# Kernel tuning notes

Measured on AMD Instinct MI355X. Metric: run time of the kernel, lower is better.

Reference implementation:

```python
import jax, jax.numpy as jnp
import numpy as np

V, E, H, L = 32000, 1024, 1024, 2  # vocab, embed, hidden, num_layers
START_TOKEN = 0


def setup_inputs() -> dict:
    key = jax.random.key(0)
    ks = jax.random.split(key, 10)
    s = 1.0 / np.sqrt(H)
    return {
        "encoder_outputs": jax.random.normal(ks[0], (64, 32, H), jnp.float32),
        "encoder_hidden": jax.random.normal(ks[1], (L, 64, H), jnp.float32),
        "emb": jax.random.normal(ks[2], (V, E), jnp.float32) * s,
        "w_ih": jax.random.normal(ks[3], (L, 3 * H, E), jnp.float32) * s,
        "w_hh": jax.random.normal(ks[4], (L, 3 * H, H), jnp.float32) * s,
        "b_ih": jax.random.normal(ks[5], (L, 3 * H), jnp.float32) * s,
        "b_hh": jax.random.normal(ks[6], (L, 3 * H), jnp.float32) * s,
        "out_w": jax.random.normal(ks[7], (V, H), jnp.float32) * s,
        "out_b": jax.random.normal(ks[8], (V,), jnp.float32) * s,
        "max_length": 32,
    }


def _gru_cell(x, h, wi, wh, bi, bh):
    # torch GRU gate order: r, z, n
    gi = x @ wi.T + bi          # [B, 3H]
    gh = h @ wh.T + bh          # [B, 3H]
    ir, iz, inn = jnp.split(gi, 3, axis=-1)
    hr, hz, hn = jnp.split(gh, 3, axis=-1)
    r = jax.nn.sigmoid(ir + hr)
    z = jax.nn.sigmoid(iz + hz)
    n = jnp.tanh(inn + r * hn)
    return (1.0 - z) * n + z * h


def reference(encoder_outputs, encoder_hidden, emb, w_ih, w_hh, b_ih, b_hh,
              out_w, out_b, max_length):
    B = encoder_outputs.shape[0]
    tok0 = jnp.full((B,), START_TOKEN, dtype=jnp.int32)

    def step(carry, _):
        h, tok = carry                      # h: [L,B,H], tok: [B]
        x = jax.nn.relu(emb[tok])           # embedding + (dropout p=0) + relu
        new_h = []
        for l in range(L):
            hl = _gru_cell(x, h[l], w_ih[l], w_hh[l], b_ih[l], b_hh[l])
            new_h.append(hl)
            x = hl
        h = jnp.stack(new_h)
        logits = x @ out_w.T + out_b        # [B, V]
        tok = jnp.argmax(logits, axis=-1).astype(jnp.int32)  # topk(1), detached
        return (h, tok), logits

    (h_final, _), logits = jax.lax.scan(step, (encoder_hidden, tok0), None,
                                        length=max_length)
    decoder_outputs = jnp.transpose(logits, (1, 0, 2))  # [B, T, V]
    return decoder_outputs, h_final
```

## Files before the change

kernel.cpp:

```cpp
#include <hip/hip_runtime.h>
#include <math.h>
#include <float.h>


#define B_ 64
#define H_ 1024
#define V_ 32000
#define T_ 32

typedef unsigned short u16;
typedef float f32x4 __attribute__((ext_vector_type(4)));
typedef short s16x8 __attribute__((ext_vector_type(8)));
#define MFMA16 __builtin_amdgcn_mfma_f32_16x16x32_bf16

#define WOH_B   0UL
#define WOL_B   65536000UL
#define WIHH_B  131072000UL
#define WIHL_B  143654912UL
#define WHHH_B  156237824UL
#define WHHL_B  168820736UL
#define XH_B    181403648UL
#define XL_B    181534720UL
#define HBH_B   181665792UL
#define HBL_B   181927936UL
#define HF_B    182190080UL
#define GT_B    182714368UL
#define PV_B    184287232UL
#define PI_B    184543232UL
#define TK_B    184799232UL

#define OUT_H_OFF 65536000L

__device__ __forceinline__ void bf16split(float x, u16& h, u16& l) {
  unsigned u = __float_as_uint(x);
  unsigned r = u + 0x7fff + ((u >> 16) & 1);
  h = (u16)(r >> 16);
  float hf = __uint_as_float((unsigned)h << 16);
  float rem = x - hf;
  unsigned u2 = __float_as_uint(rem);
  unsigned r2 = u2 + 0x7fff + ((u2 >> 16) & 1);
  l = (u16)(r2 >> 16);
}

__global__ void k_convert(const float* __restrict__ src, u16* __restrict__ hi,
                          u16* __restrict__ lo, int n4) {
  int i = blockIdx.x * 256 + threadIdx.x;
  int stride = gridDim.x * 256;
  for (; i < n4; i += stride) {
    float4 v = ((const float4*)src)[i];
    float x[4] = {v.x, v.y, v.z, v.w};
    u16 hh[4], ll[4];
    #pragma unroll
    for (int j = 0; j < 4; ++j) bf16split(x[j], hh[j], ll[j]);
    ushort4 ho; ho.x = hh[0]; ho.y = hh[1]; ho.z = hh[2]; ho.w = hh[3];
    ushort4 lv; lv.x = ll[0]; lv.y = ll[1]; lv.z = ll[2]; lv.w = ll[3];
    ((ushort4*)hi)[i] = ho;
    ((ushort4*)lo)[i] = lv;
  }
}

__global__ void k_init(const float* __restrict__ enc_h, float* __restrict__ hf,
                       u16* __restrict__ hhi, u16* __restrict__ hlo,
                       int* __restrict__ tok) {
  int n = blockIdx.x * 256 + threadIdx.x;
  float v = enc_h[n];
  hf[n] = v;
  u16 h, l; bf16split(v, h, l);
  hhi[n] = h; hlo[n] = l;
  if (n < B_) tok[n] = 0;
}

__global__ void k_argmax_embed(const float* __restrict__ emb,
                               const float* __restrict__ pv, const int* __restrict__ pidx,
                               int* __restrict__ tok, u16* __restrict__ xhi,
                               u16* __restrict__ xlo, int do_argmax) {
  __shared__ float sv[1024];
  __shared__ int   si[1024];
  int tid = threadIdx.x;
  if (do_argmax) {
    int b = tid & 63, c = tid >> 6;
    float best = -FLT_MAX; int bi = 0x7fffffff;
    for (int i = c; i < 1000; i += 16) {
      float v = pv[i * 64 + b];
      int  ix = pidx[i * 64 + b];
      if (v > best || (v == best && ix < bi)) { best = v; bi = ix; }
    }
    sv[c * 64 + b] = best; si[c * 64 + b] = bi;
    __syncthreads();
    if (tid < 64) {
      float bv = sv[tid]; int bix = si[tid];
      #pragma unroll
      for (int c2 = 1; c2 < 16; ++c2) {
        float v2 = sv[c2 * 64 + tid]; int i2 = si[c2 * 64 + tid];
        if (v2 > bv || (v2 == bv && i2 < bix)) { bv = v2; bix = i2; }
      }
      tok[tid] = bix;
    }
  }
  __syncthreads();
  int b = tid >> 4, tl = tid & 15;
  const float* erow = emb + (long)tok[b] * H_;
  #pragma unroll
  for (int c = 0; c < 16; ++c) {
    int e = c * 64 + tl * 4;
    float4 v = *(const float4*)(erow + e);
    float x0 = fmaxf(v.x, 0.f), x1 = fmaxf(v.y, 0.f);
    float x2 = fmaxf(v.z, 0.f), x3 = fmaxf(v.w, 0.f);
    u16 h0,h1,h2,h3,l0,l1,l2,l3;
    bf16split(x0,h0,l0); bf16split(x1,h1,l1); bf16split(x2,h2,l2); bf16split(x3,h3,l3);
    ushort4 hv; hv.x=h0; hv.y=h1; hv.z=h2; hv.w=h3;
    ushort4 lv; lv.x=l0; lv.y=l1; lv.z=l2; lv.w=l3;
    *(ushort4*)(xhi + b * 1024 + e) = hv;
    *(ushort4*)(xlo + b * 1024 + e) = lv;
  }
}

__device__ __forceinline__ void gemm32x64_slice(
    const u16* __restrict__ Ahi, const u16* __restrict__ Alo,
    const u16* __restrict__ Bhi, const u16* __restrict__ Blo,
    int lane, int kbeg, f32x4 (&acc)[2][4]) {
  int l15 = lane & 15, l4 = lane >> 4;
  const u16* pah = Ahi + l15 * 1024 + l4 * 8 + kbeg;
  const u16* pal = Alo + l15 * 1024 + l4 * 8 + kbeg;
  const u16* pbh = Bhi + l15 * 1024 + l4 * 8 + kbeg;
  const u16* pbl = Blo + l15 * 1024 + l4 * 8 + kbeg;
  #pragma unroll 2
  for (int k0 = 0; k0 < 256; k0 += 32) {
    s16x8 ah0 = *(const s16x8*)(pah + k0);
    s16x8 ah1 = *(const s16x8*)(pah + 16 * 1024 + k0);
    s16x8 al0 = *(const s16x8*)(pal + k0);
    s16x8 al1 = *(const s16x8*)(pal + 16 * 1024 + k0);
    #pragma unroll
    for (int nt = 0; nt < 4; ++nt) {
      s16x8 bh = *(const s16x8*)(pbh + nt * 16 * 1024 + k0);
      s16x8 bl = *(const s16x8*)(pbl + nt * 16 * 1024 + k0);
      acc[0][nt] = MFMA16(ah0, bh, acc[0][nt], 0, 0, 0);
      acc[1][nt] = MFMA16(ah1, bh, acc[1][nt], 0, 0, 0);
      acc[0][nt] = MFMA16(ah0, bl, acc[0][nt], 0, 0, 0);
      acc[1][nt] = MFMA16(ah1, bl, acc[1][nt], 0, 0, 0);
      acc[0][nt] = MFMA16(al0, bh, acc[0][nt], 0, 0, 0);
      acc[1][nt] = MFMA16(al1, bh, acc[1][nt], 0, 0, 0);
    }
  }
}

__global__ __launch_bounds__(256) void k_gru(
    const u16* __restrict__ aih_hi, const u16* __restrict__ aih_lo,
    const u16* __restrict__ ahh_hi, const u16* __restrict__ ahh_lo,
    const float* __restrict__ bih, const float* __restrict__ bhh,
    const u16* __restrict__ xb_hi, const u16* __restrict__ xb_lo,
    const u16* __restrict__ hb_hi, const u16* __restrict__ hb_lo,
    float* __restrict__ gt) {
  __shared__ f32x4 sacc[4][64][5];
  int tid = threadIdx.x;
  int wave = tid >> 6, lane = tid & 63;
  int l15 = lane & 15, l4 = lane >> 4;
  int blk = blockIdx.x;
  bool ih = blk < 96;
  int row0 = (ih ? blk : blk - 96) * 32;
  const u16* Ahi = (ih ? aih_hi : ahh_hi) + (size_t)row0 * 1024;
  const u16* Alo = (ih ? aih_lo : ahh_lo) + (size_t)row0 * 1024;
  const u16* Bhi = ih ? xb_hi : hb_hi;
  const u16* Blo = ih ? xb_lo : hb_lo;
  const float* bias = (ih ? bih : bhh) + row0;
  f32x4 acc[2][4];
  #pragma unroll
  for (int m = 0; m < 2; ++m)
    #pragma unroll
    for (int n = 0; n < 4; ++n) acc[m][n] = (f32x4){0.f, 0.f, 0.f, 0.f};
  gemm32x64_slice(Ahi, Alo, Bhi, Blo, lane, wave * 256, acc);
  #pragma unroll
  for (int nt = 0; nt < 4; ++nt) sacc[wave][lane][nt] = acc[0][nt];
  __syncthreads();
  f32x4 s0 = sacc[0][lane][wave];
  #pragma unroll
  for (int j = 1; j < 4; ++j) s0 += sacc[j][lane][wave];
  __syncthreads();
  #pragma unroll
  for (int nt = 0; nt < 4; ++nt) sacc[wave][lane][nt] = acc[1][nt];
  __syncthreads();
  f32x4 s1 = sacc[0][lane][wave];
  #pragma unroll
  for (int j = 1; j < 4; ++j) s1 += sacc[j][lane][wave];
  int grow0 = (ih ? 0 : 3072) + row0;
  int b = wave * 16 + l15;
  f32x4 bs0 = *(const f32x4*)(bias + l4 * 4);
  f32x4 bs1 = *(const f32x4*)(bias + 16 + l4 * 4);
  *(f32x4*)(gt + (size_t)b * 6144 + grow0 + l4 * 4) = s0 + bs0;
  *(f32x4*)(gt + (size_t)b * 6144 + grow0 + 16 + l4 * 4) = s1 + bs1;
}

__global__ void k_gates(const float* __restrict__ gt, float* __restrict__ hf,
                        u16* __restrict__ hhi, u16* __restrict__ hlo) {
  int n = blockIdx.x * 256 + threadIdx.x;
  int b = n >> 10, j = n & 1023;
  const float* gb = gt + (size_t)b * 6144;
  float ir = gb[j], iz = gb[j + 1024], inn = gb[j + 2048];
  float hr = gb[j + 3072], hz = gb[j + 4096], hn = gb[j + 5120];
  float r = 1.f / (1.f + expf(-(ir + hr)));
  float z = 1.f / (1.f + expf(-(iz + hz)));
  float nn = tanhf(inn + r * hn);
  float ho = hf[n];
  float hv = (1.f - z) * nn + z * ho;
  hf[n] = hv;
  u16 hh, ll; bf16split(hv, hh, ll);
  hhi[n] = hh; hlo[n] = ll;
}

__global__ __launch_bounds__(256) void k_logits(
    const u16* __restrict__ whi, const u16* __restrict__ wlo,
    const float* __restrict__ bo, const u16* __restrict__ xhi,
    const u16* __restrict__ xlo, float* __restrict__ pv, int* __restrict__ pidx,
    float* __restrict__ dout, int t) {
  __shared__ f32x4 sacc[4][64][5];
  int tid = threadIdx.x;
  int wave = tid >> 6, lane = tid & 63;
  int l15 = lane & 15, l4 = lane >> 4;
  int v0 = blockIdx.x * 32;
  f32x4 acc[2][4];
  #pragma unroll
  for (int m = 0; m < 2; ++m)
    #pragma unroll
    for (int n = 0; n < 4; ++n) acc[m][n] = (f32x4){0.f, 0.f, 0.f, 0.f};
  gemm32x64_slice(whi + (size_t)v0 * 1024, wlo + (size_t)v0 * 1024,
                  xhi, xlo, lane, wave * 256, acc);
  #pragma unroll
  for (int nt = 0; nt < 4; ++nt) sacc[wave][lane][nt] = acc[0][nt];
  __syncthreads();
  f32x4 s0 = sacc[0][lane][wave];
  #pragma unroll
  for (int j = 1; j < 4; ++j) s0 += sacc[j][lane][wave];
  __syncthreads();
  #pragma unroll
  for (int nt = 0; nt < 4; ++nt) sacc[wave][lane][nt] = acc[1][nt];
  __syncthreads();
  f32x4 s1 = sacc[0][lane][wave];
  #pragma unroll
  for (int j = 1; j < 4; ++j) s1 += sacc[j][lane][wave];
  long b = wave * 16 + l15;
  f32x4 out0 = s0 + *(const f32x4*)(bo + v0 + l4 * 4);
  f32x4 out1 = s1 + *(const f32x4*)(bo + v0 + 16 + l4 * 4);
  float* addr = dout + b * (T_ * (long)V_) + (long)t * V_ + v0 + l4 * 4;
  __builtin_nontemporal_store(out0, (f32x4*)addr);
  __builtin_nontemporal_store(out1, (f32x4*)(addr + 16));
  float bv = -FLT_MAX; int bi = 0;
  #pragma unroll
  for (int r = 0; r < 4; ++r) {
    float v = out0[r];
    if (v > bv) { bv = v; bi = v0 + l4 * 4 + r; }
  }
  #pragma unroll
  for (int r = 0; r < 4; ++r) {
    float v = out1[r];
    if (v > bv) { bv = v; bi = v0 + 16 + l4 * 4 + r; }
  }
  #pragma unroll
  for (int off = 16; off < 64; off <<= 1) {
    float ov = __shfl_xor(bv, off, 64);
    int   oi = __shfl_xor(bi, off, 64);
    if (ov > bv || (ov == bv && oi < bi)) { bv = ov; bi = oi; }
  }
  if (l4 == 0) {
    pv[blockIdx.x * 64 + wave * 16 + l15] = bv;
    pidx[blockIdx.x * 64 + wave * 16 + l15] = bi;
  }
}

__global__ void k_final(const float* __restrict__ hf, float* __restrict__ dout) {
  int n = blockIdx.x * 256 + threadIdx.x;
  dout[OUT_H_OFF + n] = hf[n];
}

extern "C" void kernel_launch(void* const* d_in, const int* in_sizes, int n_in,
                              void* d_out, int out_size, void* d_ws, size_t ws_size,
                              hipStream_t stream) {
  const float* enc_h = (const float*)d_in[1];
  const float* emb   = (const float*)d_in[2];
  const float* w_ih  = (const float*)d_in[3];
  const float* w_hh  = (const float*)d_in[4];
  const float* b_ih  = (const float*)d_in[5];
  const float* b_hh  = (const float*)d_in[6];
  const float* out_w = (const float*)d_in[7];
  const float* out_b = (const float*)d_in[8];
  float* out = (float*)d_out;
  char* wsb = (char*)d_ws;

  u16* woh  = (u16*)(wsb + WOH_B);
  u16* wol  = (u16*)(wsb + WOL_B);
  u16* wihh = (u16*)(wsb + WIHH_B);
  u16* wihl = (u16*)(wsb + WIHL_B);
  u16* whhh = (u16*)(wsb + WHHH_B);
  u16* whhl = (u16*)(wsb + WHHL_B);
  u16* xh   = (u16*)(wsb + XH_B);
  u16* xl   = (u16*)(wsb + XL_B);
  u16* hbh  = (u16*)(wsb + HBH_B);
  u16* hbl  = (u16*)(wsb + HBL_B);
  float* hf = (float*)(wsb + HF_B);
  float* gt = (float*)(wsb + GT_B);
  float* pv = (float*)(wsb + PV_B);
  int* pidx = (int*)(wsb + PI_B);
  int* tok  = (int*)(wsb + TK_B);

  k_convert<<<4096, 256, 0, stream>>>(out_w, woh, wol, 8192000);
  k_convert<<<2048, 256, 0, stream>>>(w_ih, wihh, wihl, 1572864);
  k_convert<<<2048, 256, 0, stream>>>(w_hh, whhh, whhl, 1572864);
  k_init<<<512, 256, 0, stream>>>(enc_h, hf, hbh, hbl, tok);

  for (int t = 0; t < T_; ++t) {
    k_argmax_embed<<<1, 1024, 0, stream>>>(emb, pv, pidx, tok, xh, xl, t > 0);
    for (int l = 0; l < 2; ++l) {
      const u16* bxh = (l == 0) ? xh : hbh;
      const u16* bxl = (l == 0) ? xl : hbl;
      k_gru<<<192, 256, 0, stream>>>(wihh + (size_t)l * 3145728, wihl + (size_t)l * 3145728,
                                     whhh + (size_t)l * 3145728, whhl + (size_t)l * 3145728,
                                     b_ih + l * 3072, b_hh + l * 3072,
                                     bxh, bxl, hbh + l * 65536, hbl + l * 65536, gt);
      k_gates<<<256, 256, 0, stream>>>(gt, hf + l * 65536, hbh + l * 65536, hbl + l * 65536);
    }
    k_logits<<<1000, 256, 0, stream>>>(woh, wol, out_b, hbh + 65536, hbl + 65536,
                                       pv, pidx, out, t);
  }
  k_final<<<512, 256, 0, stream>>>(hf, out);
}
```

Before: 3.794 ms.

## Stage weight tiles into LDS via global_load_lds with 8-wave K split

The GEMM helper is restructured so each of 8 waves (512 threads) handles a 128-wide K slice. Each wave preloads its activation fragments into registers and streams the weight tile (hi and lo) directly into LDS with global_load_lds before running the MFMAs. The cross-wave reduction becomes a single 8-way LDS sum done by the first 4 waves. The goal is more bytes in flight per block and less latency for the bandwidth-bound weight streaming. In exchange each block uses 128 KB of LDS, which caps occupancy at one block per CU, and register pressure rises from the 32 preloaded B fragments.

New measurement: 4.001 ms. 5.5% more time.

```diff
diff --git a/kernel.cpp b/kernel.cpp
--- a/kernel.cpp
+++ b/kernel.cpp
@@ -42,6 +42,12 @@
   l = (u16)(r2 >> 16);
 }
 
+__device__ __forceinline__ void ld_g2l(void* lptr, const void* gptr) {
+  __builtin_amdgcn_global_load_lds(
+      (const __attribute__((address_space(1))) void*)gptr,
+      (__attribute__((address_space(3))) void*)lptr, 16, 0, 0);
+}
+
 __global__ void k_convert(const float* __restrict__ src, u16* __restrict__ hi,
                           u16* __restrict__ lo, int n4) {
   int i = blockIdx.x * 256 + threadIdx.x;
@@ -80,6 +86,7 @@
   if (do_argmax) {
     int b = tid & 63, c = tid >> 6;
     float best = -FLT_MAX; int bi = 0x7fffffff;
+    #pragma unroll 4
     for (int i = c; i < 1000; i += 16) {
       float v = pv[i * 64 + b];
       int  ix = pidx[i * 64 + b];
@@ -115,51 +122,65 @@
   }
 }
 
-__device__ __forceinline__ void gemm32x64_slice(
+__device__ __forceinline__ void stage_gemm32x64(
     const u16* __restrict__ Ahi, const u16* __restrict__ Alo,
     const u16* __restrict__ Bhi, const u16* __restrict__ Blo,
-    int lane, int kbeg, f32x4 (&acc)[2][4]) {
+    char* wslice, int wave, int lane, f32x4 (&acc)[2][4]) {
   int l15 = lane & 15, l4 = lane >> 4;
-  const u16* pah = Ahi + l15 * 1024 + l4 * 8 + kbeg;
-  const u16* pal = Alo + l15 * 1024 + l4 * 8 + kbeg;
-  const u16* pbh = Bhi + l15 * 1024 + l4 * 8 + kbeg;
-  const u16* pbl = Blo + l15 * 1024 + l4 * 8 + kbeg;
-  #pragma unroll 2
-  for (int k0 = 0; k0 < 256; k0 += 32) {
-    s16x8 ah0 = *(const s16x8*)(pah + k0);
-    s16x8 ah1 = *(const s16x8*)(pah + 16 * 1024 + k0);
-    s16x8 al0 = *(const s16x8*)(pal + k0);
-    s16x8 al1 = *(const s16x8*)(pal + 16 * 1024 + k0);
+  const u16* pbh = Bhi + l15 * 1024 + l4 * 8 + wave * 128;
+  const u16* pbl = Blo + l15 * 1024 + l4 * 8 + wave * 128;
+  s16x8 bh[4][4], bl[4][4];
+  #pragma unroll
+  for (int c = 0; c < 4; ++c)
     #pragma unroll
     for (int nt = 0; nt < 4; ++nt) {
-      s16x8 bh = *(const s16x8*)(pbh + nt * 16 * 1024 + k0);
-      s16x8 bl = *(const s16x8*)(pbl + nt * 16 * 1024 + k0);
-      acc[0][nt] = MFMA16(ah0, bh, acc[0][nt], 0, 0, 0);
-      acc[1][nt] = MFMA16(ah1, bh, acc[1][nt], 0, 0, 0);
-      acc[0][nt] = MFMA16(ah0, bl, acc[0][nt], 0, 0, 0);
-      acc[1][nt] = MFMA16(ah1, bl, acc[1][nt], 0, 0, 0);
-      acc[0][nt] = MFMA16(al0, bh, acc[0][nt], 0, 0, 0);
-      acc[1][nt] = MFMA16(al1, bh, acc[1][nt], 0, 0, 0);
-    }
-  }
-}
-
-__global__ __launch_bounds__(256) void k_gru(
+      bh[c][nt] = *(const s16x8*)(pbh + nt * 16384 + c * 32);
+      bl[c][nt] = *(const s16x8*)(pbl + nt * 16384 + c * 32);
+    }
+  {
+    int row = (lane >> 4);
+    int kof = (lane & 15) * 8;
+    #pragma unroll
+    for (int i = 0; i < 8; ++i) {
+      ld_g2l(wslice + i * 1024,        Ahi + (size_t)(i * 4 + row) * 1024 + kof);
+      ld_g2l(wslice + 8192 + i * 1024, Alo + (size_t)(i * 4 + row) * 1024 + kof);
+    }
+  }
+  __syncthreads();
+  #pragma unroll
+  for (int c = 0; c < 4; ++c) {
+    s16x8 ah0 = *(const s16x8*)(wslice + l15 * 256 + c * 64 + l4 * 16);
+    s16x8 ah1 = *(const s16x8*)(wslice + (l15 + 16) * 256 + c * 64 + l4 * 16);
+    s16x8 al0 = *(const s16x8*)(wslice + 8192 + l15 * 256 + c * 64 + l4 * 16);
+    s16x8 al1 = *(const s16x8*)(wslice + 8192 + (l15 + 16) * 256 + c * 64 + l4 * 16);
+    #pragma unroll
+    for (int nt = 0; nt < 4; ++nt) {
+      acc[0][nt] = MFMA16(ah0, bh[c][nt], acc[0][nt], 0, 0, 0);
+      acc[1][nt] = MFMA16(ah1, bh[c][nt], acc[1][nt], 0, 0, 0);
+      acc[0][nt] = MFMA16(ah0, bl[c][nt], acc[0][nt], 0, 0, 0);
+      acc[1][nt] = MFMA16(ah1, bl[c][nt], acc[1][nt], 0, 0, 0);
+      acc[0][nt] = MFMA16(al0, bh[c][nt], acc[0][nt], 0, 0, 0);
+      acc[1][nt] = MFMA16(al1, bh[c][nt], acc[1][nt], 0, 0, 0);
+    }
+  }
+}
+
+__global__ __launch_bounds__(512) void k_gru(
     const u16* __restrict__ aih_hi, const u16* __restrict__ aih_lo,
     const u16* __restrict__ ahh_hi, const u16* __restrict__ ahh_lo,
     const float* __restrict__ bih, const float* __restrict__ bhh,
     const u16* __restrict__ xb_hi, const u16* __restrict__ xb_lo,
     const u16* __restrict__ hb_hi, const u16* __restrict__ hb_lo,
     float* __restrict__ gt) {
-  __shared__ f32x4 sacc[4][64][5];
+  __shared__ __align__(16) char lds[131072];
   int tid = threadIdx.x;
   int wave = tid >> 6, lane = tid & 63;
   int l15 = lane & 15, l4 = lane >> 4;
   int blk = blockIdx.x;
   bool ih = blk < 96;
   int row0 = (ih ? blk : blk - 96) * 32;
-  const u16* Ahi = (ih ? aih_hi : ahh_hi) + (size_t)row0 * 1024;
-  const u16* Alo = (ih ? aih_lo : ahh_lo) + (size_t)row0 * 1024;
+  const u16* Ahi = (ih ? aih_hi : ahh_hi) + (size_t)row0 * 1024 + wave * 128;
+  const u16* Alo = (ih ? aih_lo : ahh_lo) + (size_t)row0 * 1024 + wave * 128;
   const u16* Bhi = ih ? xb_hi : hb_hi;
   const u16* Blo = ih ? xb_lo : hb_lo;
   const float* bias = (ih ? bih : bhh) + row0;
@@ -168,26 +189,30 @@
   for (int m = 0; m < 2; ++m)
     #pragma unroll
     for (int n = 0; n < 4; ++n) acc[m][n] = (f32x4){0.f, 0.f, 0.f, 0.f};
-  gemm32x64_slice(Ahi, Alo, Bhi, Blo, lane, wave * 256, acc);
-  #pragma unroll
-  for (int nt = 0; nt < 4; ++nt) sacc[wave][lane][nt] = acc[0][nt];
-  __syncthreads();
-  f32x4 s0 = sacc[0][lane][wave];
-  #pragma unroll
-  for (int j = 1; j < 4; ++j) s0 += sacc[j][lane][wave];
-  __syncthreads();
-  #pragma unroll
-  for (int nt = 0; nt < 4; ++nt) sacc[wave][lane][nt] = acc[1][nt];
-  __syncthreads();
-  f32x4 s1 = sacc[0][lane][wave];
-  #pragma unroll
-  for (int j = 1; j < 4; ++j) s1 += sacc[j][lane][wave];
-  int grow0 = (ih ? 0 : 3072) + row0;
-  int b = wave * 16 + l15;
-  f32x4 bs0 = *(const f32x4*)(bias + l4 * 4);
-  f32x4 bs1 = *(const f32x4*)(bias + 16 + l4 * 4);
-  *(f32x4*)(gt + (size_t)b * 6144 + grow0 + l4 * 4) = s0 + bs0;
-  *(f32x4*)(gt + (size_t)b * 6144 + grow0 + 16 + l4 * 4) = s1 + bs1;
+  stage_gemm32x64(Ahi, Alo, Bhi, Blo, lds + wave * 16384, wave, lane, acc);
+  __syncthreads();
+  f32x4* sa = (f32x4*)lds;
+  #pragma unroll
+  for (int mt = 0; mt < 2; ++mt)
+    #pragma unroll
+    for (int nt = 0; nt < 4; ++nt)
+      sa[(mt * 4 + nt) * 512 + wave * 64 + lane] = acc[mt][nt];
+  __syncthreads();
+  if (wave < 4) {
+    f32x4 s0 = sa[wave * 512 + lane];
+    f32x4 s1 = sa[(4 + wave) * 512 + lane];
+    #pragma unroll
+    for (int j = 1; j < 8; ++j) {
+      s0 += sa[wave * 512 + j * 64 + lane];
+      s1 += sa[(4 + wave) * 512 + j * 64 + lane];
+    }
+    int grow0 = (ih ? 0 : 3072) + row0;
+    int b = wave * 16 + l15;
+    f32x4 bs0 = *(const f32x4*)(bias + l4 * 4);
+    f32x4 bs1 = *(const f32x4*)(bias + 16 + l4 * 4);
+    *(f32x4*)(gt + (size_t)b * 6144 + grow0 + l4 * 4) = s0 + bs0;
+    *(f32x4*)(gt + (size_t)b * 6144 + grow0 + 16 + l4 * 4) = s1 + bs1;
+  }
 }
 
 __global__ void k_gates(const float* __restrict__ gt, float* __restrict__ hf,
@@ -207,12 +232,12 @@
   hhi[n] = hh; hlo[n] = ll;
 }
 
-__global__ __launch_bounds__(256) void k_logits(
+__global__ __launch_bounds__(512) void k_logits(
     const u16* __restrict__ whi, const u16* __restrict__ wlo,
     const float* __restrict__ bo, const u16* __restrict__ xhi,
     const u16* __restrict__ xlo, float* __restrict__ pv, int* __restrict__ pidx,
     float* __restrict__ dout, int t) {
-  __shared__ f32x4 sacc[4][64][5];
+  __shared__ __align__(16) char lds[131072];
   int tid = threadIdx.x;
   int wave = tid >> 6, lane = tid & 63;
   int l15 = lane & 15, l4 = lane >> 4;
@@ -222,47 +247,52 @@
   for (int m = 0; m < 2; ++m)
     #pragma unroll
     for (int n = 0; n < 4; ++n) acc[m][n] = (f32x4){0.f, 0.f, 0.f, 0.f};
-  gemm32x64_slice(whi + (size_t)v0 * 1024, wlo + (size_t)v0 * 1024,
-                  xhi, xlo, lane, wave * 256, acc);
-  #pragma unroll
-  for (int nt = 0; nt < 4; ++nt) sacc[wave][lane][nt] = acc[0][nt];
-  __syncthreads();
-  f32x4 s0 = sacc[0][lane][wave];
-  #pragma unroll
-  for (int j = 1; j < 4; ++j) s0 += sacc[j][lane][wave];
-  __syncthreads();
-  #pragma unroll
-  for (int nt = 0; nt < 4; ++nt) sacc[wave][lane][nt] = acc[1][nt];
-  __syncthreads();
-  f32x4 s1 = sacc[0][lane][wave];
-  #pragma unroll
-  for (int j = 1; j < 4; ++j) s1 += sacc[j][lane][wave];
-  long b = wave * 16 + l15;
-  f32x4 out0 = s0 + *(const f32x4*)(bo + v0 + l4 * 4);
-  f32x4 out1 = s1 + *(const f32x4*)(bo + v0 + 16 + l4 * 4);
-  float* addr = dout + b * (T_ * (long)V_) + (long)t * V_ + v0 + l4 * 4;
-  __builtin_nontemporal_store(out0, (f32x4*)addr);
-  __builtin_nontemporal_store(out1, (f32x4*)(addr + 16));
-  float bv = -FLT_MAX; int bi = 0;
-  #pragma unroll
-  for (int r = 0; r < 4; ++r) {
-    float v = out0[r];
-    if (v > bv) { bv = v; bi = v0 + l4 * 4 + r; }
-  }
-  #pragma unroll
-  for (int r = 0; r < 4; ++r) {
-    float v = out1[r];
-    if (v > bv) { bv = v; bi = v0 + 16 + l4 * 4 + r; }
-  }
-  #pragma unroll
-  for (int off = 16; off < 64; off <<= 1) {
-    float ov = __shfl_xor(bv, off, 64);
-    int   oi = __shfl_xor(bi, off, 64);
-    if (ov > bv || (ov == bv && oi < bi)) { bv = ov; bi = oi; }
-  }
-  if (l4 == 0) {
-    pv[blockIdx.x * 64 + wave * 16 + l15] = bv;
-    pidx[blockIdx.x * 64 + wave * 16 + l15] = bi;
+  stage_gemm32x64(whi + (size_t)v0 * 1024 + wave * 128,
+                  wlo + (size_t)v0 * 1024 + wave * 128,
+                  xhi, xlo, lds + wave * 16384, wave, lane, acc);
+  __syncthreads();
+  f32x4* sa = (f32x4*)lds;
+  #pragma unroll
+  for (int mt = 0; mt < 2; ++mt)
+    #pragma unroll
+    for (int nt = 0; nt < 4; ++nt)
+      sa[(mt * 4 + nt) * 512 + wave * 64 + lane] = acc[mt][nt];
+  __syncthreads();
+  if (wave < 4) {
+    f32x4 s0 = sa[wave * 512 + lane];
+    f32x4 s1 = sa[(4 + wave) * 512 + lane];
+    #pragma unroll
+    for (int j = 1; j < 8; ++j) {
+      s0 += sa[wave * 512 + j * 64 + lane];
+      s1 += sa[(4 + wave) * 512 + j * 64 + lane];
+    }
+    long b = wave * 16 + l15;
+    f32x4 out0 = s0 + *(const f32x4*)(bo + v0 + l4 * 4);
+    f32x4 out1 = s1 + *(const f32x4*)(bo + v0 + 16 + l4 * 4);
+    float* addr = dout + b * (T_ * (long)V_) + (long)t * V_ + v0 + l4 * 4;
+    __builtin_nontemporal_store(out0, (f32x4*)addr);
+    __builtin_nontemporal_store(out1, (f32x4*)(addr + 16));
+    float bv = -FLT_MAX; int bi = 0;
+    #pragma unroll
+    for (int r = 0; r < 4; ++r) {
+      float v = out0[r];
+      if (v > bv) { bv = v; bi = v0 + l4 * 4 + r; }
+    }
+    #pragma unroll
+    for (int r = 0; r < 4; ++r) {
+      float v = out1[r];
+      if (v > bv) { bv = v; bi = v0 + 16 + l4 * 4 + r; }
+    }
+    #pragma unroll
+    for (int off = 16; off < 64; off <<= 1) {
+      float ov = __shfl_xor(bv, off, 64);
+      int   oi = __shfl_xor(bi, off, 64);
+      if (ov > bv || (ov == bv && oi < bi)) { bv = ov; bi = oi; }
+    }
+    if (l4 == 0) {
+      pv[blockIdx.x * 64 + wave * 16 + l15] = bv;
+      pidx[blockIdx.x * 64 + wave * 16 + l15] = bi;
+    }
   }
 }
 
@@ -311,13 +341,13 @@
     for (int l = 0; l < 2; ++l) {
       const u16* bxh = (l == 0) ? xh : hbh;
       const u16* bxl = (l == 0) ? xl : hbl;
-      k_gru<<<192, 256, 0, stream>>>(wihh + (size_t)l * 3145728, wihl + (size_t)l * 3145728,
+      k_gru<<<192, 512, 0, stream>>>(wihh + (size_t)l * 3145728, wihl + (size_t)l * 3145728,
                                      whhh + (size_t)l * 3145728, whhl + (size_t)l * 3145728,
                                      b_ih + l * 3072, b_hh + l * 3072,
                                      bxh, bxl, hbh + l * 65536, hbl + l * 65536, gt);
       k_gates<<<256, 256, 0, stream>>>(gt, hf + l * 65536, hbh + l * 65536, hbl + l * 65536);
     }
-    k_logits<<<1000, 256, 0, stream>>>(woh, wol, out_b, hbh + 65536, hbl + 65536,
+    k_logits<<<1000, 512, 0, stream>>>(woh, wol, out_b, hbh + 65536, hbl + 65536,
                                        pv, pidx, out, t);
   }
   k_final<<<512, 256, 0, stream>>>(hf, out);
```
